# Kernel optimization log

Measured on AMD Instinct MI355X. Metric: run time of the kernel, lower is better.

## Reference

```python
import jax, jax.numpy as jnp
import numpy as np

B, M, H, NH = 64, 512, 1024, 8
HD = H // NH
EPS = 1e-5


def setup_inputs() -> dict:
    key = jax.random.key(0)
    ks = jax.random.split(key, 16)
    def n(k, shape, s=0.02):
        return jax.random.normal(k, shape, dtype=jnp.float32) * s
    z = lambda shape: jnp.zeros(shape, jnp.float32)
    return {
        "x": jax.random.normal(ks[0], (B, M, M), dtype=jnp.float32),
        # 1x1 Conv2d(1->H): weight [H,1,1,1] flattened to [H], plus bias [H]
        "conv_w": n(ks[1], (H,)), "conv_b": n(ks[2], (H,)),
        # MLP: Linear(M->H), ReLU, Linear(H->H); weights stored [in,out]
        "w1": n(ks[3], (M, H)), "b1": z((H,)),
        "w2": n(ks[4], (H, H)), "b2": z((H,)),
        "ln_g": jnp.ones((H,), jnp.float32), "ln_b": z((H,)),
        "wq": n(ks[5], (H, H)), "bq": z((H,)),
        "wk": n(ks[6], (H, H)), "bk": z((H,)),
        "wv": n(ks[7], (H, H)), "bv": z((H,)),
        "wo": n(ks[8], (H, H)), "bo": z((H,)),
        "wp": n(ks[9], (H, H)), "bp": z((H,)),
    }


def reference(x, conv_w, conv_b, w1, b1, w2, b2, ln_g, ln_b,
              wq, bq, wk, bk, wv, bv, wo, bo, wp, bp):
    # RegionConvolution: 1x1 conv over 1 input channel to H channels, then
    # mean over channels. Since mean_c(x*w_c + b_c) = x*mean(w) + mean(b),
    # compute the reduced affine form (identical math, no [B,H,M,M] temp).
    x = x + (x * conv_w.mean() + conv_b.mean())          # residual conv add, [B,M,M]
    # RegionEmbeddingMLP
    x_reg = jnp.maximum(x @ w1 + b1, 0.0) @ w2 + b2      # [B,M,H]
    # LayerNorm
    mu = x_reg.mean(-1, keepdims=True)
    var = ((x_reg - mu) ** 2).mean(-1, keepdims=True)
    x_norm = (x_reg - mu) / jnp.sqrt(var + EPS) * ln_g + ln_b
    # MHSA with multiplicative off-diagonal mask (diagonal scores zeroed)
    def heads(y):
        return y.reshape(B, M, NH, HD).transpose(0, 2, 1, 3)  # [B,NH,M,HD]
    q = heads(x_norm @ wq + bq)
    k = heads(x_norm @ wk + bk)
    v = heads(x_norm @ wv + bv)
    scores = jnp.einsum('bhqd,bhkd->bhqk', q, k) / jnp.sqrt(jnp.float32(HD))
    scores = scores * (1.0 - jnp.eye(M, dtype=scores.dtype))  # zero diagonal
    attn = jax.nn.softmax(scores, axis=-1)
    ctx = jnp.einsum('bhqk,bhkd->bhqd', attn, v)
    ctx = ctx.transpose(0, 2, 1, 3).reshape(B, M, H)
    attn_out = ctx @ wo + bo
    attn_out = attn_out @ wp + bp                        # output_proj
    return attn_out + x_reg                              # residual, [B,M,H]
```

## Files before the change

### kernel.cpp

```cpp
#include <hip/hip_runtime.h>
#include <hip/hip_fp16.h>
#include <cstdint>
#include <cstddef>

typedef _Float16 f16;
typedef _Float16 f16x8 __attribute__((ext_vector_type(8)));
typedef _Float16 f16x4 __attribute__((ext_vector_type(4)));
typedef float f32x4 __attribute__((ext_vector_type(4)));

#define NB 64
#define SEQ 512
#define HDIM 1024
#define NHEAD 8
#define HD 128
#define MR (NB * SEQ)
#define QK_LD 2048

__device__ __forceinline__ void async_copy16(const f16* g, f16* l) {
  __builtin_amdgcn_global_load_lds(
      (__attribute__((address_space(1))) void*)(void*)const_cast<f16*>(g),
      (__attribute__((address_space(3))) void*)l, 16, 0, 0);
}


__global__ __launch_bounds__(256) void conv_reduce(
    const float* __restrict__ cw, const float* __restrict__ cb,
    float* __restrict__ out2) {
  int t = threadIdx.x;
  float a = 0.f, b = 0.f;
  for (int i = t; i < HDIM; i += 256) { a += cw[i]; b += cb[i]; }
  for (int m = 32; m >= 1; m >>= 1) { a += __shfl_xor(a, m); b += __shfl_xor(b, m); }
  __shared__ float sa[4], sb[4];
  if ((t & 63) == 0) { sa[t >> 6] = a; sb[t >> 6] = b; }
  __syncthreads();
  if (t == 0) {
    out2[0] = (sa[0] + sa[1] + sa[2] + sa[3]) * (1.f / HDIM);
    out2[1] = (sb[0] + sb[1] + sb[2] + sb[3]) * (1.f / HDIM);
  }
}

__global__ __launch_bounds__(256) void prep_x(
    const float* __restrict__ x, const float* __restrict__ cs,
    f16* __restrict__ xh) {
  size_t i = (size_t)blockIdx.x * 256 + threadIdx.x;
  float cw = 1.f + cs[0], cb = cs[1];
  float4 v = ((const float4*)x)[i];
  f16x4 o;
  o[0] = (f16)(v.x * cw + cb);
  o[1] = (f16)(v.y * cw + cb);
  o[2] = (f16)(v.z * cw + cb);
  o[3] = (f16)(v.w * cw + cb);
  ((f16x4*)xh)[i] = o;
}

__global__ __launch_bounds__(256) void concat_bias(
    const float* __restrict__ bq, const float* __restrict__ bk,
    const float* __restrict__ bv, float* __restrict__ dst) {
  int i = blockIdx.x * 256 + threadIdx.x;
  if (i < 1024) dst[i] = bq[i];
  else if (i < 2048) dst[i] = bk[i - 1024];
  else dst[i] = bv[i - 2048];
}

__global__ __launch_bounds__(256) void cast_f16(
    const float* __restrict__ src, f16* __restrict__ dst) {
  size_t i = (size_t)blockIdx.x * 256 + threadIdx.x;
  float4 v = ((const float4*)src)[i];
  f16x4 o;
  o[0] = (f16)v.x; o[1] = (f16)v.y; o[2] = (f16)v.z; o[3] = (f16)v.w;
  ((f16x4*)dst)[i] = o;
}

__global__ __launch_bounds__(256) void fuse_bias_p1(
    const float* __restrict__ bo, const float* __restrict__ wp,
    float* __restrict__ partial) {
  int n = blockIdx.x * 256 + threadIdx.x;
  int jc = blockIdx.y;
  float s = 0.f;
#pragma unroll 8
  for (int j = jc * 128; j < jc * 128 + 128; j++) s += bo[j] * wp[(size_t)j * 1024 + n];
  partial[(size_t)jc * 1024 + n] = s;
}

__global__ __launch_bounds__(256) void fuse_bias_p2(
    const float* __restrict__ partial, const float* __restrict__ bp,
    float* __restrict__ bp2) {
  int n = blockIdx.x * 256 + threadIdx.x;
  float s = bp[n];
#pragma unroll
  for (int jc = 0; jc < 8; jc++) s += partial[(size_t)jc * 1024 + n];
  bp2[n] = s;
}

__global__ __launch_bounds__(256) void transpose_cast(
    const float* __restrict__ src, f16* __restrict__ dst, int K, int N) {
  __shared__ float tile[32][33];
  int tx = threadIdx.x, ty = threadIdx.y;
  int n0 = blockIdx.x * 32, k0 = blockIdx.y * 32;
#pragma unroll
  for (int r = 0; r < 32; r += 8) tile[ty + r][tx] = src[(size_t)(k0 + ty + r) * N + n0 + tx];
  __syncthreads();
#pragma unroll
  for (int r = 0; r < 32; r += 8)
    dst[(size_t)(n0 + ty + r) * K + k0 + tx] = (f16)tile[tx][ty + r];
}

__global__ __launch_bounds__(256) void transpose_cast5(
    const float* s0, const float* s1, const float* s2, const float* s3, const float* s4,
    f16* d0, f16* d1, f16* d2, f16* d3, f16* d4) {
  const float* src; f16* dst;
  switch (blockIdx.z) {
    case 0: src = s0; dst = d0; break;
    case 1: src = s1; dst = d1; break;
    case 2: src = s2; dst = d2; break;
    case 3: src = s3; dst = d3; break;
    default: src = s4; dst = d4; break;
  }
  __shared__ float tile[32][33];
  int tx = threadIdx.x, ty = threadIdx.y;
  int n0 = blockIdx.x * 32, k0 = blockIdx.y * 32;
#pragma unroll
  for (int r = 0; r < 32; r += 8) tile[ty + r][tx] = src[(size_t)(k0 + ty + r) * 1024 + n0 + tx];
  __syncthreads();
#pragma unroll
  for (int r = 0; r < 32; r += 8)
    dst[(size_t)(n0 + ty + r) * 1024 + k0 + tx] = (f16)tile[tx][ty + r];
}

__global__ __launch_bounds__(256) void ln_kernel(
    const f16* __restrict__ xin, const float* __restrict__ g,
    const float* __restrict__ bta, f16* __restrict__ out) {
  int row = blockIdx.x;
  int t = threadIdx.x;
  f16x4 vh = ((const f16x4*)(xin + (size_t)row * HDIM))[t];
  float vx = (float)vh[0], vy = (float)vh[1], vz = (float)vh[2], vw = (float)vh[3];
  float s = vx + vy + vz + vw;
  float s2 = vx * vx + vy * vy + vz * vz + vw * vw;
  for (int m = 32; m >= 1; m >>= 1) { s += __shfl_xor(s, m); s2 += __shfl_xor(s2, m); }
  __shared__ float sa[4], sb[4];
  if ((t & 63) == 0) { sa[t >> 6] = s; sb[t >> 6] = s2; }
  __syncthreads();
  float S = sa[0] + sa[1] + sa[2] + sa[3];
  float S2 = sb[0] + sb[1] + sb[2] + sb[3];
  float mu = S * (1.f / HDIM);
  float var = S2 * (1.f / HDIM) - mu * mu;
  float inv = rsqrtf(var + 1e-5f);
  float4 gv = ((const float4*)g)[t];
  float4 bv = ((const float4*)bta)[t];
  f16x4 o;
  o[0] = (f16)((vx - mu) * inv * gv.x + bv.x);
  o[1] = (f16)((vy - mu) * inv * gv.y + bv.y);
  o[2] = (f16)((vz - mu) * inv * gv.z + bv.z);
  o[3] = (f16)((vw - mu) * inv * gv.w + bv.w);
  ((f16x4*)(out + (size_t)row * HDIM))[t] = o;
}

template <int EPI>
__global__ __launch_bounds__(512) void gemm_nt(
    const f16* __restrict__ A, const f16* __restrict__ BT,
    const float* __restrict__ bias, void* __restrict__ Cout, int N, int K,
    const f16* __restrict__ Xres, f16* __restrict__ vTout) {
  __shared__ __align__(16) f16 As[128 * 64];
  __shared__ __align__(16) f16 Bs[128 * 64];
  const int tid = threadIdx.x;
  const int wave = tid >> 6, lane = tid & 63;
  const int l15 = lane & 15, quad = lane >> 4;

  const int gn = N >> 7;
  const int gm = (int)gridDim.x / gn;
  const int pid = blockIdx.x;
  const int npg = 16 * gn;
  const int gid = pid / npg;
  const int rem = pid - gid * npg;
  const int grows = min(16, gm - gid * 16);
  const int bm = gid * 16 + rem % grows;
  const int bn = rem / grows;

  const int wm = wave >> 2, wn = wave & 3;

  f32x4 z4 = {0.f, 0.f, 0.f, 0.f};
  f32x4 acc[4][2];
#pragma unroll
  for (int i = 0; i < 4; i++)
#pragma unroll
    for (int j = 0; j < 2; j++) acc[i][j] = z4;

  const int srow = tid >> 3;
  const int c = ((tid & 7) - (srow & 7)) & 7;
  const f16* Ag = A + (size_t)(bm * 128 + srow) * K + c * 8;
  const f16* Bg = BT + (size_t)(bn * 128 + srow) * K + c * 8;
  f16* Al0 = As + tid * 8;
  f16* Al1 = As + 64 * 64 + tid * 8;
  f16* Bl0 = Bs + tid * 8;
  f16* Bl1 = Bs + 64 * 64 + tid * 8;
  const size_t kstep = (size_t)64 * K;

  const int r7 = l15 & 7;

  for (int k0 = 0; k0 < K; k0 += 64) {
    async_copy16(Ag, Al0);
    async_copy16(Ag + kstep, Al1);
    async_copy16(Bg, Bl0);
    async_copy16(Bg + kstep, Bl1);
    Ag += 64; Bg += 64;
    __syncthreads();
#pragma unroll
    for (int s = 0; s < 2; s++) {
      f16x8 af[4], bfr[2];
#pragma unroll
      for (int t = 0; t < 4; t++) {
        int phys = (s * 4 + quad + r7) & 7;
        af[t] = *(const f16x8*)&As[(wm * 64 + t * 16 + l15) * 64 + phys * 8];
      }
#pragma unroll
      for (int u = 0; u < 2; u++) {
        int phys = (s * 4 + quad + r7) & 7;
        bfr[u] = *(const f16x8*)&Bs[(wn * 32 + u * 16 + l15) * 64 + phys * 8];
      }
#pragma unroll
      for (int i = 0; i < 4; i++)
#pragma unroll
        for (int j = 0; j < 2; j++)
          acc[i][j] = __builtin_amdgcn_mfma_f32_16x16x32_f16(af[i], bfr[j], acc[i][j], 0, 0, 0);
    }
    __syncthreads();
  }

  float* Cf = (float*)Cout;
  f16* Ch = (f16*)Cout;
#pragma unroll
  for (int i = 0; i < 4; i++) {
    int r0 = bm * 128 + wm * 64 + i * 16 + quad * 4;
#pragma unroll
    for (int j = 0; j < 2; j++) {
      int c0 = bn * 128 + wn * 32 + j * 16;
      int cc = c0 + l15;
      float bv = (EPI == 4) ? 0.f : bias[cc];
      if (EPI == 6 && c0 >= 2048) {
        int hh = (cc - 2048) >> 7, d = (cc - 2048) & 127;
        int bb = r0 >> 9, ml = r0 & 511;
        f16x4 o;
#pragma unroll
        for (int reg = 0; reg < 4; reg++) o[reg] = (f16)(acc[i][j][reg] + bv);
        *(f16x4*)&vTout[((size_t)(bb * NHEAD + hh) * HD + d) * SEQ + ml] = o;
      } else {
#pragma unroll
        for (int reg = 0; reg < 4; reg++) {
          float v = acc[i][j][reg] + bv;
          if (EPI == 0)      Ch[(size_t)(r0 + reg) * N + cc] = (f16)fmaxf(v, 0.f);
          else if (EPI == 1) Ch[(size_t)(r0 + reg) * N + cc] = (f16)v;
          else if (EPI == 4) Ch[(size_t)(r0 + reg) * N + cc] = (f16)v;
          else if (EPI == 5) {
            size_t idx = (size_t)(r0 + reg) * N + cc;
            Cf[idx] = v + (float)Xres[idx];
          } else {
            Ch[(size_t)(r0 + reg) * QK_LD + cc] = (f16)v;
          }
        }
      }
    }
  }
}

__global__ __launch_bounds__(512) void attn_kernel(
    const f16* __restrict__ qkv, const f16* __restrict__ vT,
    f16* __restrict__ ctx) {
  const int tid = threadIdx.x;
  const int wave = tid >> 6, lane = tid & 63;
  const int l15 = lane & 15, quad = lane >> 4;
  const int bidx = blockIdx.x;
  const int qc = bidx >> 9;
  const int bh = bidx & 511;
  const int h = bh & 7, bb = bh >> 3;

  const f16* Qbase = qkv + (size_t)(bb * SEQ) * QK_LD + h * 128;
  const f16* Kbase = Qbase + 1024;
  const f16* VTbase = vT + (size_t)(bb * NHEAD + h) * HD * SEQ;

  __shared__ __align__(16) f16 Ks[64 * 128];
  __shared__ __align__(16) f16 VTs[128 * 64];
  __shared__ __align__(16) f16 Ps[8 * 32 * 72];

  const float scale = 0.08838834764831845f;
  const int qrow0 = qc * 256 + wave * 32;
  f16x8 qf[2][4];
#pragma unroll
  for (int tm = 0; tm < 2; tm++)
#pragma unroll
    for (int s = 0; s < 4; s++) {
      qf[tm][s] = *(const f16x8*)(Qbase + (size_t)(qrow0 + tm * 16 + l15) * QK_LD + s * 32 + quad * 8);
#pragma unroll
      for (int e = 0; e < 8; e++) qf[tm][s][e] *= (f16)scale;
    }

  f32x4 z4 = {0.f, 0.f, 0.f, 0.f};
  f32x4 O[2][8];
#pragma unroll
  for (int i = 0; i < 2; i++)
#pragma unroll
    for (int j = 0; j < 8; j++) O[i][j] = z4;
  float lrow[2][4];
#pragma unroll
  for (int i = 0; i < 2; i++)
#pragma unroll
    for (int r = 0; r < 4; r++) lrow[i][r] = 0.f;

  const int kc = ((tid & 15) - ((tid >> 4) & 15)) & 15;
  const f16* Kg = Kbase + (size_t)(tid >> 4) * QK_LD + kc * 8;
  f16* Kl = Ks + tid * 8;
  const int vc = ((tid & 7) - ((tid >> 3) & 7)) & 7;
  const f16* Vg = VTbase + (size_t)(tid >> 3) * SEQ + vc * 8;
  f16* Vl = VTs + tid * 8;

  f16* Pw = &Ps[wave * 32 * 72];
  const int r7 = l15 & 7;

  for (int kt = 0; kt < 8; kt++) {
    const int krow0 = kt * 64;
#pragma unroll
    for (int i = 0; i < 2; i++)
      async_copy16(Kg + (size_t)(krow0 + 32 * i) * QK_LD, Kl + 4096 * i);
#pragma unroll
    for (int i = 0; i < 2; i++)
      async_copy16(Vg + (size_t)(64 * i) * SEQ + krow0, Vl + 4096 * i);
    __syncthreads();

    f32x4 S[2][4];
#pragma unroll
    for (int i = 0; i < 2; i++)
#pragma unroll
      for (int j = 0; j < 4; j++) S[i][j] = z4;
#pragma unroll
    for (int s = 0; s < 4; s++) {
      f16x8 bfr[4];
#pragma unroll
      for (int tn = 0; tn < 4; tn++) {
        int phys = (s * 4 + quad + l15) & 15;
        bfr[tn] = *(const f16x8*)&Ks[(tn * 16 + l15) * 128 + phys * 8];
      }
#pragma unroll
      for (int tm = 0; tm < 2; tm++)
#pragma unroll
        for (int tn = 0; tn < 4; tn++)
          S[tm][tn] = __builtin_amdgcn_mfma_f32_16x16x32_f16(qf[tm][s], bfr[tn], S[tm][tn], 0, 0, 0);
    }

#pragma unroll
    for (int tm = 0; tm < 2; tm++) {
#pragma unroll
      for (int reg = 0; reg < 4; reg++) {
        int qg = qrow0 + tm * 16 + quad * 4 + reg;
        float rs = 0.f;
#pragma unroll
        for (int tn = 0; tn < 4; tn++) {
          int kg = krow0 + tn * 16 + l15;
          float p = (kg == qg) ? 1.f : __expf(S[tm][tn][reg]);
          S[tm][tn][reg] = p;
          rs += p;
        }
        rs += __shfl_xor(rs, 1); rs += __shfl_xor(rs, 2);
        rs += __shfl_xor(rs, 4); rs += __shfl_xor(rs, 8);
        lrow[tm][reg] += rs;
      }
    }

#pragma unroll
    for (int tm = 0; tm < 2; tm++)
#pragma unroll
      for (int reg = 0; reg < 4; reg++)
#pragma unroll
        for (int tn = 0; tn < 4; tn++)
          Pw[(tm * 16 + quad * 4 + reg) * 72 + tn * 16 + l15] = (f16)S[tm][tn][reg];
    asm volatile("s_waitcnt lgkmcnt(0)" ::: "memory");

#pragma unroll
    for (int ks = 0; ks < 2; ks++) {
      f16x8 pa[2];
#pragma unroll
      for (int tm = 0; tm < 2; tm++)
        pa[tm] = *(const f16x8*)&Pw[(tm * 16 + l15) * 72 + ks * 32 + quad * 8];
#pragma unroll
      for (int tn = 0; tn < 8; tn++) {
        int phys = (ks * 4 + quad + r7) & 7;
        f16x8 vb = *(const f16x8*)&VTs[(tn * 16 + l15) * 64 + phys * 8];
#pragma unroll
        for (int tm = 0; tm < 2; tm++)
          O[tm][tn] = __builtin_amdgcn_mfma_f32_16x16x32_f16(pa[tm], vb, O[tm][tn], 0, 0, 0);
      }
    }
    __syncthreads();
  }

#pragma unroll
  for (int tm = 0; tm < 2; tm++)
#pragma unroll
    for (int reg = 0; reg < 4; reg++) {
      float inv = 1.f / lrow[tm][reg];
      int row = bb * SEQ + qrow0 + tm * 16 + quad * 4 + reg;
#pragma unroll
      for (int tn = 0; tn < 8; tn++) {
        int col = h * 128 + tn * 16 + l15;
        ctx[(size_t)row * HDIM + col] = (f16)(O[tm][tn][reg] * inv);
      }
    }
}


extern "C" void kernel_launch(void* const* d_in, const int* in_sizes, int n_in,
                              void* d_out, int out_size, void* d_ws, size_t ws_size,
                              hipStream_t stream) {
  (void)in_sizes; (void)n_in; (void)out_size; (void)ws_size;
  const float* x      = (const float*)d_in[0];
  const float* conv_w = (const float*)d_in[1];
  const float* conv_b = (const float*)d_in[2];
  const float* w1     = (const float*)d_in[3];
  const float* b1     = (const float*)d_in[4];
  const float* w2     = (const float*)d_in[5];
  const float* b2     = (const float*)d_in[6];
  const float* ln_g   = (const float*)d_in[7];
  const float* ln_b   = (const float*)d_in[8];
  const float* wq     = (const float*)d_in[9];
  const float* bq     = (const float*)d_in[10];
  const float* wk     = (const float*)d_in[11];
  const float* bk     = (const float*)d_in[12];
  const float* wv     = (const float*)d_in[13];
  const float* bv     = (const float*)d_in[14];
  const float* wo     = (const float*)d_in[15];
  const float* bo     = (const float*)d_in[16];
  const float* wp     = (const float*)d_in[17];
  const float* bp     = (const float*)d_in[18];
  float* out = (float*)d_out;

  char* ws = (char*)d_ws;
  size_t off = 0;
  auto alloc = [&](size_t bytes) {
    char* p = ws + off;
    off += (bytes + 255) & ~(size_t)255;
    return p;
  };
  float* cs    = (float*)alloc(8);
  f16* w1T     = (f16*)alloc((size_t)1024 * 512 * 2);
  f16* w2T     = (f16*)alloc((size_t)1024 * 1024 * 2);
  f16* qkvT    = (f16*)alloc((size_t)3072 * 1024 * 2);
  f16* wpT     = (f16*)alloc((size_t)1024 * 1024 * 2);
  f16* woh     = (f16*)alloc((size_t)1024 * 1024 * 2);
  f16* woPT    = (f16*)alloc((size_t)1024 * 1024 * 2);
  float* bqkv  = (float*)alloc((size_t)3072 * 4);
  float* bp2   = (float*)alloc((size_t)1024 * 4);
  float* part  = (float*)alloc((size_t)8 * 1024 * 4);
  f16* qkvQK   = (f16*)alloc((size_t)MR * QK_LD * 2);
  f16* h1      = (f16*)alloc((size_t)MR * 1024 * 2);
  f16* x_norm  = (f16*)alloc((size_t)MR * 1024 * 2);
  f16* x_regh  = (f16*)alloc((size_t)MR * 1024 * 2);
  f16* xh = qkvQK;
  f16* vT = h1;
  f16* ctx = x_norm;

  dim3 tb(32, 8);
  conv_reduce<<<1, 256, 0, stream>>>(conv_w, conv_b, cs);
  transpose_cast<<<dim3(32, 16), tb, 0, stream>>>(w1, w1T, 512, 1024);
  transpose_cast5<<<dim3(32, 32, 5), tb, 0, stream>>>(
      w2, wq, wk, wv, wp,
      w2T, qkvT, qkvT + (size_t)1024 * 1024, qkvT + (size_t)2048 * 1024, wpT);
  cast_f16<<<1024, 256, 0, stream>>>(wo, woh);
  concat_bias<<<12, 256, 0, stream>>>(bq, bk, bv, bqkv);
  fuse_bias_p1<<<dim3(4, 8), 256, 0, stream>>>(bo, wp, part);
  fuse_bias_p2<<<4, 256, 0, stream>>>(part, bp, bp2);
  prep_x<<<16384, 256, 0, stream>>>(x, cs, xh);

  gemm_nt<4><<<dim3(64), 512, 0, stream>>>(wpT, woh, nullptr, (void*)woPT, 1024, 1024, nullptr, nullptr);

  gemm_nt<0><<<dim3(256 * 8), 512, 0, stream>>>(xh, w1T, b1, (void*)h1, 1024, 512, nullptr, nullptr);
  gemm_nt<1><<<dim3(256 * 8), 512, 0, stream>>>(h1, w2T, b2, (void*)x_regh, 1024, 1024, nullptr, nullptr);
  ln_kernel<<<32768, 256, 0, stream>>>(x_regh, ln_g, ln_b, x_norm);
  gemm_nt<6><<<dim3(256 * 24), 512, 0, stream>>>(x_norm, qkvT, bqkv, (void*)qkvQK, 3072, 1024, nullptr, vT);
  attn_kernel<<<1024, 512, 0, stream>>>(qkvQK, vT, ctx);
  gemm_nt<5><<<dim3(256 * 8), 512, 0, stream>>>(ctx, woPT, bp2, (void*)out, 1024, 1024, x_regh, nullptr);
}
```

Before: 896.8 us.

## Add 256x256-tile pipelined GEMM kernel with XCD-aware block remap for main GEMMs

```diff
diff --git a/kernel.cpp b/kernel.cpp
--- a/kernel.cpp
+++ b/kernel.cpp
@@ -226,7 +226,6 @@
     __syncthreads();
   }
 
-  float* Cf = (float*)Cout;
   f16* Ch = (f16*)Cout;
 #pragma unroll
   for (int i = 0; i < 4; i++) {
@@ -236,6 +235,132 @@
       int c0 = bn * 128 + wn * 32 + j * 16;
       int cc = c0 + l15;
       float bv = (EPI == 4) ? 0.f : bias[cc];
+#pragma unroll
+      for (int reg = 0; reg < 4; reg++) {
+        float v = acc[i][j][reg] + bv;
+        Ch[(size_t)(r0 + reg) * N + cc] = (f16)v;
+      }
+    }
+  }
+  (void)Xres; (void)vTout;
+}
+
+template <int EPI>
+__global__ __launch_bounds__(512, 2) void gemm256(
+    const f16* __restrict__ A, const f16* __restrict__ BT,
+    const float* __restrict__ bias, void* __restrict__ Cout, int N, int K,
+    const f16* __restrict__ Xres, f16* __restrict__ vTout) {
+  __shared__ __align__(16) f16 As[4 * 8192];
+  __shared__ __align__(16) f16 Bs[4 * 8192];
+  const int tid = threadIdx.x;
+  const int wave = tid >> 6, lane = tid & 63;
+  const int l15 = lane & 15, quad = lane >> 4;
+  const int wm = wave >> 2, wn = wave & 3;
+
+  const int nbn = N >> 8;
+  const int nwg = (int)gridDim.x;
+  const int wg = (blockIdx.x & 7) * (nwg >> 3) + (blockIdx.x >> 3);
+  const int bm = wg / nbn, bn = wg - bm * nbn;
+
+  const int srow = tid >> 2;
+  const int sq = ((tid & 3) - (srow >> 1)) & 3;
+  const f16* Ag = A + (size_t)(bm * 256 + srow) * K + sq * 8;
+  const f16* Bg = BT + (size_t)(bn * 256 + srow) * K + sq * 8;
+  const size_t rstep = (size_t)128 * K;
+  const int rphys = ((quad + (l15 >> 1)) & 3) * 8;
+
+#define STAGE_A_(BUF, S, K0) do {                                      \
+    const f16* g_ = Ag + (K0) + (S) * 32;                              \
+    f16* l_ = As + ((BUF) * 2 + (S)) * 8192 + tid * 8;                 \
+    async_copy16(g_, l_); async_copy16(g_ + rstep, l_ + 4096); } while (0)
+#define STAGE_B_(BUF, S, K0) do {                                      \
+    const f16* g_ = Bg + (K0) + (S) * 32;                              \
+    f16* l_ = Bs + ((BUF) * 2 + (S)) * 8192 + tid * 8;                 \
+    async_copy16(g_, l_); async_copy16(g_ + rstep, l_ + 4096); } while (0)
+#define READ_A_(DST, BUF, S, RG) do {                                  \
+    _Pragma("unroll") for (int i_ = 0; i_ < 4; i_++)                   \
+      DST[i_] = *(const f16x8*)&As[((BUF) * 2 + (S)) * 8192 +          \
+          (wm * 128 + (RG) * 64 + i_ * 16 + l15) * 32 + rphys];        \
+  } while (0)
+#define READ_B_(DST, BUF, S) do {                                      \
+    _Pragma("unroll") for (int j_ = 0; j_ < 4; j_++)                   \
+      DST[j_] = *(const f16x8*)&Bs[((BUF) * 2 + (S)) * 8192 +          \
+          (wn * 64 + j_ * 16 + l15) * 32 + rphys];                     \
+  } while (0)
+#define MFMA16_(RG, AF, BF) do {                                       \
+    _Pragma("unroll") for (int i_ = 0; i_ < 4; i_++)                   \
+      _Pragma("unroll") for (int j_ = 0; j_ < 4; j_++)                 \
+        acc[(RG) * 4 + i_][j_] = __builtin_amdgcn_mfma_f32_16x16x32_f16( \
+            AF[i_], BF[j_], acc[(RG) * 4 + i_][j_], 0, 0, 0);          \
+  } while (0)
+#define BAR_() __builtin_amdgcn_s_barrier()
+#define LGKM0_() asm volatile("s_waitcnt lgkmcnt(0)" ::: "memory")
+#define VMC4_() asm volatile("s_waitcnt vmcnt(4)" ::: "memory")
+#define VMC0_() asm volatile("s_waitcnt vmcnt(0)" ::: "memory")
+
+  f32x4 z4 = {0.f, 0.f, 0.f, 0.f};
+  f32x4 acc[8][4];
+#pragma unroll
+  for (int i = 0; i < 8; i++)
+#pragma unroll
+    for (int j = 0; j < 4; j++) acc[i][j] = z4;
+
+  STAGE_A_(0, 0, 0); STAGE_B_(0, 0, 0); STAGE_A_(0, 1, 0); STAGE_B_(0, 1, 0);
+  VMC4_();
+  BAR_();
+
+  const int NT = K >> 6;
+  for (int t = 0; t < NT; ++t) {
+    const int buf = t & 1, bufn = buf ^ 1;
+    const int k1 = (t + 1) << 6;
+    const bool pf = (t + 1) < NT;
+    f16x8 af[4], bf0[4], bf1[4];
+
+    READ_A_(af, buf, 0, 0);
+    READ_B_(bf0, buf, 0);
+    if (pf) STAGE_A_(bufn, 0, k1);
+    BAR_(); LGKM0_();
+    __builtin_amdgcn_s_setprio(1);
+    MFMA16_(0, af, bf0);
+    __builtin_amdgcn_s_setprio(0);
+    BAR_();
+
+    READ_A_(af, buf, 0, 1);
+    if (pf) { STAGE_B_(bufn, 0, k1); VMC4_(); } else { VMC0_(); }
+    BAR_(); LGKM0_();
+    __builtin_amdgcn_s_setprio(1);
+    MFMA16_(1, af, bf0);
+    __builtin_amdgcn_s_setprio(0);
+    BAR_();
+
+    READ_A_(af, buf, 1, 0);
+    READ_B_(bf1, buf, 1);
+    if (pf) STAGE_A_(bufn, 1, k1);
+    BAR_(); LGKM0_();
+    __builtin_amdgcn_s_setprio(1);
+    MFMA16_(0, af, bf1);
+    __builtin_amdgcn_s_setprio(0);
+    BAR_();
+
+    READ_A_(af, buf, 1, 1);
+    if (pf) { STAGE_B_(bufn, 1, k1); VMC4_(); }
+    BAR_(); LGKM0_();
+    __builtin_amdgcn_s_setprio(1);
+    MFMA16_(1, af, bf1);
+    __builtin_amdgcn_s_setprio(0);
+    BAR_();
+  }
+
+  float* Cf = (float*)Cout;
+  f16* Ch = (f16*)Cout;
+#pragma unroll
+  for (int i = 0; i < 8; i++) {
+    int r0 = bm * 256 + wm * 128 + i * 16 + quad * 4;
+#pragma unroll
+    for (int j = 0; j < 4; j++) {
+      int c0 = bn * 256 + wn * 64 + j * 16;
+      int cc = c0 + l15;
+      float bv = bias[cc];
       if (EPI == 6 && c0 >= 2048) {
         int hh = (cc - 2048) >> 7, d = (cc - 2048) & 127;
         int bb = r0 >> 9, ml = r0 & 511;
@@ -249,7 +374,6 @@
           float v = acc[i][j][reg] + bv;
           if (EPI == 0)      Ch[(size_t)(r0 + reg) * N + cc] = (f16)fmaxf(v, 0.f);
           else if (EPI == 1) Ch[(size_t)(r0 + reg) * N + cc] = (f16)v;
-          else if (EPI == 4) Ch[(size_t)(r0 + reg) * N + cc] = (f16)v;
           else if (EPI == 5) {
             size_t idx = (size_t)(r0 + reg) * N + cc;
             Cf[idx] = v + (float)Xres[idx];
@@ -260,6 +384,15 @@
       }
     }
   }
+#undef STAGE_A_
+#undef STAGE_B_
+#undef READ_A_
+#undef READ_B_
+#undef MFMA16_
+#undef BAR_
+#undef LGKM0_
+#undef VMC4_
+#undef VMC0_
 }
 
 __global__ __launch_bounds__(512) void attn_kernel(
@@ -470,10 +603,10 @@
 
   gemm_nt<4><<<dim3(64), 512, 0, stream>>>(wpT, woh, nullptr, (void*)woPT, 1024, 1024, nullptr, nullptr);
 
-  gemm_nt<0><<<dim3(256 * 8), 512, 0, stream>>>(xh, w1T, b1, (void*)h1, 1024, 512, nullptr, nullptr);
-  gemm_nt<1><<<dim3(256 * 8), 512, 0, stream>>>(h1, w2T, b2, (void*)x_regh, 1024, 1024, nullptr, nullptr);
+  gemm256<0><<<dim3(128 * 4), 512, 0, stream>>>(xh, w1T, b1, (void*)h1, 1024, 512, nullptr, nullptr);
+  gemm256<1><<<dim3(128 * 4), 512, 0, stream>>>(h1, w2T, b2, (void*)x_regh, 1024, 1024, nullptr, nullptr);
   ln_kernel<<<32768, 256, 0, stream>>>(x_regh, ln_g, ln_b, x_norm);
-  gemm_nt<6><<<dim3(256 * 24), 512, 0, stream>>>(x_norm, qkvT, bqkv, (void*)qkvQK, 3072, 1024, nullptr, vT);
+  gemm256<6><<<dim3(128 * 12), 512, 0, stream>>>(x_norm, qkvT, bqkv, (void*)qkvQK, 3072, 1024, nullptr, vT);
   attn_kernel<<<1024, 512, 0, stream>>>(qkvQK, vT, ctx);
-  gemm_nt<5><<<dim3(256 * 8), 512, 0, stream>>>(ctx, woPT, bp2, (void*)out, 1024, 1024, x_regh, nullptr);
-}
+  gemm256<5><<<dim3(128 * 4), 512, 0, stream>>>(ctx, woPT, bp2, (void*)out, 1024, 1024, x_regh, nullptr);
+}
```

Result: no change. 881.9 us (-1.7%).

## Use 4-wave 64x64 warp tiles in GEMM, split QKV GEMM, add MFMA priority

Applied to the files above, without the earlier changes.

```diff
diff --git a/kernel.cpp b/kernel.cpp
--- a/kernel.cpp
+++ b/kernel.cpp
@@ -156,7 +156,7 @@
 }
 
 template <int EPI>
-__global__ __launch_bounds__(512) void gemm_nt(
+__global__ __launch_bounds__(256) void gemm_nt(
     const f16* __restrict__ A, const f16* __restrict__ BT,
     const float* __restrict__ bias, void* __restrict__ Cout, int N, int K,
     const f16* __restrict__ Xres, f16* __restrict__ vTout) {
@@ -176,51 +176,44 @@
   const int bm = gid * 16 + rem % grows;
   const int bn = rem / grows;
 
-  const int wm = wave >> 2, wn = wave & 3;
+  const int wm = wave >> 1, wn = wave & 1;
 
   f32x4 z4 = {0.f, 0.f, 0.f, 0.f};
-  f32x4 acc[4][2];
+  f32x4 acc[4][4];
 #pragma unroll
   for (int i = 0; i < 4; i++)
 #pragma unroll
-    for (int j = 0; j < 2; j++) acc[i][j] = z4;
+    for (int j = 0; j < 4; j++) acc[i][j] = z4;
 
   const int srow = tid >> 3;
   const int c = ((tid & 7) - (srow & 7)) & 7;
   const f16* Ag = A + (size_t)(bm * 128 + srow) * K + c * 8;
   const f16* Bg = BT + (size_t)(bn * 128 + srow) * K + c * 8;
-  f16* Al0 = As + tid * 8;
-  f16* Al1 = As + 64 * 64 + tid * 8;
-  f16* Bl0 = Bs + tid * 8;
-  f16* Bl1 = Bs + 64 * 64 + tid * 8;
-  const size_t kstep = (size_t)64 * K;
+  const size_t kstep32 = (size_t)32 * K;
 
   const int r7 = l15 & 7;
 
   for (int k0 = 0; k0 < K; k0 += 64) {
-    async_copy16(Ag, Al0);
-    async_copy16(Ag + kstep, Al1);
-    async_copy16(Bg, Bl0);
-    async_copy16(Bg + kstep, Bl1);
+#pragma unroll
+    for (int i = 0; i < 4; i++) async_copy16(Ag + i * kstep32, As + i * 2048 + tid * 8);
+#pragma unroll
+    for (int i = 0; i < 4; i++) async_copy16(Bg + i * kstep32, Bs + i * 2048 + tid * 8);
     Ag += 64; Bg += 64;
     __syncthreads();
 #pragma unroll
     for (int s = 0; s < 2; s++) {
-      f16x8 af[4], bfr[2];
-#pragma unroll
-      for (int t = 0; t < 4; t++) {
-        int phys = (s * 4 + quad + r7) & 7;
+      const int phys = (s * 4 + quad + r7) & 7;
+      f16x8 af[4], bfr[4];
+#pragma unroll
+      for (int t = 0; t < 4; t++)
         af[t] = *(const f16x8*)&As[(wm * 64 + t * 16 + l15) * 64 + phys * 8];
-      }
-#pragma unroll
-      for (int u = 0; u < 2; u++) {
-        int phys = (s * 4 + quad + r7) & 7;
-        bfr[u] = *(const f16x8*)&Bs[(wn * 32 + u * 16 + l15) * 64 + phys * 8];
-      }
+#pragma unroll
+      for (int u = 0; u < 4; u++)
+        bfr[u] = *(const f16x8*)&Bs[(wn * 64 + u * 16 + l15) * 64 + phys * 8];
 #pragma unroll
       for (int i = 0; i < 4; i++)
 #pragma unroll
-        for (int j = 0; j < 2; j++)
+        for (int j = 0; j < 4; j++)
           acc[i][j] = __builtin_amdgcn_mfma_f32_16x16x32_f16(af[i], bfr[j], acc[i][j], 0, 0, 0);
     }
     __syncthreads();
@@ -232,12 +225,12 @@
   for (int i = 0; i < 4; i++) {
     int r0 = bm * 128 + wm * 64 + i * 16 + quad * 4;
 #pragma unroll
-    for (int j = 0; j < 2; j++) {
-      int c0 = bn * 128 + wn * 32 + j * 16;
+    for (int j = 0; j < 4; j++) {
+      int c0 = bn * 128 + wn * 64 + j * 16;
       int cc = c0 + l15;
       float bv = (EPI == 4) ? 0.f : bias[cc];
-      if (EPI == 6 && c0 >= 2048) {
-        int hh = (cc - 2048) >> 7, d = (cc - 2048) & 127;
+      if (EPI == 7) {
+        int hh = cc >> 7, d = cc & 127;
         int bb = r0 >> 9, ml = r0 & 511;
         f16x4 o;
 #pragma unroll
@@ -253,8 +246,6 @@
           else if (EPI == 5) {
             size_t idx = (size_t)(r0 + reg) * N + cc;
             Cf[idx] = v + (float)Xres[idx];
-          } else {
-            Ch[(size_t)(r0 + reg) * QK_LD + cc] = (f16)v;
           }
         }
       }
@@ -338,11 +329,13 @@
         int phys = (s * 4 + quad + l15) & 15;
         bfr[tn] = *(const f16x8*)&Ks[(tn * 16 + l15) * 128 + phys * 8];
       }
+      __builtin_amdgcn_s_setprio(1);
 #pragma unroll
       for (int tm = 0; tm < 2; tm++)
 #pragma unroll
         for (int tn = 0; tn < 4; tn++)
           S[tm][tn] = __builtin_amdgcn_mfma_f32_16x16x32_f16(qf[tm][s], bfr[tn], S[tm][tn], 0, 0, 0);
+      __builtin_amdgcn_s_setprio(0);
     }
 
 #pragma unroll
@@ -379,6 +372,7 @@
 #pragma unroll
       for (int tm = 0; tm < 2; tm++)
         pa[tm] = *(const f16x8*)&Pw[(tm * 16 + l15) * 72 + ks * 32 + quad * 8];
+      __builtin_amdgcn_s_setprio(1);
 #pragma unroll
       for (int tn = 0; tn < 8; tn++) {
         int phys = (ks * 4 + quad + r7) & 7;
@@ -387,6 +381,7 @@
         for (int tm = 0; tm < 2; tm++)
           O[tm][tn] = __builtin_amdgcn_mfma_f32_16x16x32_f16(pa[tm], vb, O[tm][tn], 0, 0, 0);
       }
+      __builtin_amdgcn_s_setprio(0);
     }
     __syncthreads();
   }
@@ -468,12 +463,14 @@
   fuse_bias_p2<<<4, 256, 0, stream>>>(part, bp, bp2);
   prep_x<<<16384, 256, 0, stream>>>(x, cs, xh);
 
-  gemm_nt<4><<<dim3(64), 512, 0, stream>>>(wpT, woh, nullptr, (void*)woPT, 1024, 1024, nullptr, nullptr);
-
-  gemm_nt<0><<<dim3(256 * 8), 512, 0, stream>>>(xh, w1T, b1, (void*)h1, 1024, 512, nullptr, nullptr);
-  gemm_nt<1><<<dim3(256 * 8), 512, 0, stream>>>(h1, w2T, b2, (void*)x_regh, 1024, 1024, nullptr, nullptr);
+  gemm_nt<4><<<dim3(64), 256, 0, stream>>>(wpT, woh, nullptr, (void*)woPT, 1024, 1024, nullptr, nullptr);
+
+  gemm_nt<0><<<dim3(256 * 8), 256, 0, stream>>>(xh, w1T, b1, (void*)h1, 1024, 512, nullptr, nullptr);
+  gemm_nt<1><<<dim3(256 * 8), 256, 0, stream>>>(h1, w2T, b2, (void*)x_regh, 1024, 1024, nullptr, nullptr);
   ln_kernel<<<32768, 256, 0, stream>>>(x_regh, ln_g, ln_b, x_norm);
-  gemm_nt<6><<<dim3(256 * 24), 512, 0, stream>>>(x_norm, qkvT, bqkv, (void*)qkvQK, 3072, 1024, nullptr, vT);
+  gemm_nt<1><<<dim3(256 * 16), 256, 0, stream>>>(x_norm, qkvT, bqkv, (void*)qkvQK, 2048, 1024, nullptr, nullptr);
+  gemm_nt<7><<<dim3(256 * 8), 256, 0, stream>>>(x_norm, qkvT + (size_t)2048 * 1024, bqkv + 2048,
+                                                nullptr, 1024, 1024, nullptr, vT);
   attn_kernel<<<1024, 512, 0, stream>>>(qkvQK, vT, ctx);
-  gemm_nt<5><<<dim3(256 * 8), 512, 0, stream>>>(ctx, woPT, bp2, (void*)out, 1024, 1024, x_regh, nullptr);
-}
+  gemm_nt<5><<<dim3(256 * 8), 256, 0, stream>>>(ctx, woPT, bp2, (void*)out, 1024, 1024, x_regh, nullptr);
+}
```

Result: slower. 916.7 us (+2.2%).

## Compute transposed QK scores and pass P to PV MFMA via register permutes

Applied to the files above, without the earlier changes.

```diff
diff --git a/kernel.cpp b/kernel.cpp
--- a/kernel.cpp
+++ b/kernel.cpp
@@ -6,7 +6,9 @@
 typedef _Float16 f16;
 typedef _Float16 f16x8 __attribute__((ext_vector_type(8)));
 typedef _Float16 f16x4 __attribute__((ext_vector_type(4)));
+typedef _Float16 f16x2 __attribute__((ext_vector_type(2)));
 typedef float f32x4 __attribute__((ext_vector_type(4)));
+typedef unsigned int ui4 __attribute__((ext_vector_type(4)));
 
 #define NB 64
 #define SEQ 512
@@ -279,7 +281,6 @@
 
   __shared__ __align__(16) f16 Ks[64 * 128];
   __shared__ __align__(16) f16 VTs[128 * 64];
-  __shared__ __align__(16) f16 Ps[8 * 32 * 72];
 
   const float scale = 0.08838834764831845f;
   const int qrow0 = qc * 256 + wave * 32;
@@ -299,11 +300,7 @@
   for (int i = 0; i < 2; i++)
 #pragma unroll
     for (int j = 0; j < 8; j++) O[i][j] = z4;
-  float lrow[2][4];
-#pragma unroll
-  for (int i = 0; i < 2; i++)
-#pragma unroll
-    for (int r = 0; r < 4; r++) lrow[i][r] = 0.f;
+  float lrow[2] = {0.f, 0.f};
 
   const int kc = ((tid & 15) - ((tid >> 4) & 15)) & 15;
   const f16* Kg = Kbase + (size_t)(tid >> 4) * QK_LD + kc * 8;
@@ -312,8 +309,8 @@
   const f16* Vg = VTbase + (size_t)(tid >> 3) * SEQ + vc * 8;
   f16* Vl = VTs + tid * 8;
 
-  f16* Pw = &Ps[wave * 32 * 72];
   const int r7 = l15 & 7;
+  const bool qodd = (quad & 1) != 0;
 
   for (int kt = 0; kt < 8; kt++) {
     const int krow0 = kt * 64;
@@ -325,11 +322,11 @@
       async_copy16(Vg + (size_t)(64 * i) * SEQ + krow0, Vl + 4096 * i);
     __syncthreads();
 
-    f32x4 S[2][4];
-#pragma unroll
-    for (int i = 0; i < 2; i++)
-#pragma unroll
-      for (int j = 0; j < 4; j++) S[i][j] = z4;
+    f32x4 ST[4][2];
+#pragma unroll
+    for (int i = 0; i < 4; i++)
+#pragma unroll
+      for (int j = 0; j < 2; j++) ST[i][j] = z4;
 #pragma unroll
     for (int s = 0; s < 4; s++) {
       f16x8 bfr[4];
@@ -338,55 +335,73 @@
         int phys = (s * 4 + quad + l15) & 15;
         bfr[tn] = *(const f16x8*)&Ks[(tn * 16 + l15) * 128 + phys * 8];
       }
-#pragma unroll
-      for (int tm = 0; tm < 2; tm++)
-#pragma unroll
-        for (int tn = 0; tn < 4; tn++)
-          S[tm][tn] = __builtin_amdgcn_mfma_f32_16x16x32_f16(qf[tm][s], bfr[tn], S[tm][tn], 0, 0, 0);
-    }
-
+      __builtin_amdgcn_s_setprio(1);
+#pragma unroll
+      for (int tn = 0; tn < 4; tn++)
+#pragma unroll
+        for (int tm = 0; tm < 2; tm++)
+          ST[tn][tm] = __builtin_amdgcn_mfma_f32_16x16x32_f16(bfr[tn], qf[tm][s], ST[tn][tm], 0, 0, 0);
+      __builtin_amdgcn_s_setprio(0);
+    }
+
+    f16x8 pa[2][2];
 #pragma unroll
     for (int tm = 0; tm < 2; tm++) {
-#pragma unroll
-      for (int reg = 0; reg < 4; reg++) {
-        int qg = qrow0 + tm * 16 + quad * 4 + reg;
-        float rs = 0.f;
-#pragma unroll
-        for (int tn = 0; tn < 4; tn++) {
-          int kg = krow0 + tn * 16 + l15;
-          float p = (kg == qg) ? 1.f : __expf(S[tm][tn][reg]);
-          S[tm][tn][reg] = p;
-          rs += p;
+      const int qg = qrow0 + tm * 16 + l15;
+      float rs = 0.f;
+      unsigned int H[4][2];
+#pragma unroll
+      for (int tn = 0; tn < 4; tn++) {
+        float p[4];
+#pragma unroll
+        for (int reg = 0; reg < 4; reg++) {
+          int kg = krow0 + tn * 16 + quad * 4 + reg;
+          float v = (kg == qg) ? 1.f : __expf(ST[tn][tm][reg]);
+          p[reg] = v;
+          rs += v;
         }
-        rs += __shfl_xor(rs, 1); rs += __shfl_xor(rs, 2);
-        rs += __shfl_xor(rs, 4); rs += __shfl_xor(rs, 8);
-        lrow[tm][reg] += rs;
-      }
-    }
-
-#pragma unroll
-    for (int tm = 0; tm < 2; tm++)
-#pragma unroll
-      for (int reg = 0; reg < 4; reg++)
-#pragma unroll
-        for (int tn = 0; tn < 4; tn++)
-          Pw[(tm * 16 + quad * 4 + reg) * 72 + tn * 16 + l15] = (f16)S[tm][tn][reg];
-    asm volatile("s_waitcnt lgkmcnt(0)" ::: "memory");
+        f16x2 h01 = {(f16)p[0], (f16)p[1]};
+        f16x2 h23 = {(f16)p[2], (f16)p[3]};
+        H[tn][0] = __builtin_bit_cast(unsigned int, h01);
+        H[tn][1] = __builtin_bit_cast(unsigned int, h23);
+      }
+      rs += __shfl_xor(rs, 16);
+      rs += __shfl_xor(rs, 32);
+      lrow[tm] += rs;
+
+#pragma unroll
+      for (int ks = 0; ks < 2; ks++) {
+        unsigned int a0 = H[ks * 2][0], a1 = H[ks * 2][1];
+        unsigned int b0 = H[ks * 2 + 1][0], b1 = H[ks * 2 + 1][1];
+        asm volatile("s_nop 1\n\tv_permlane32_swap_b32 %0, %1\n\ts_nop 1"
+                     : "+v"(a0), "+v"(b0));
+        asm volatile("s_nop 1\n\tv_permlane32_swap_b32 %0, %1\n\ts_nop 1"
+                     : "+v"(a1), "+v"(b1));
+        unsigned int c0 = (unsigned int)__shfl_xor((int)a0, 16);
+        unsigned int c1 = (unsigned int)__shfl_xor((int)a1, 16);
+        unsigned int d0 = (unsigned int)__shfl_xor((int)b0, 16);
+        unsigned int d1 = (unsigned int)__shfl_xor((int)b1, 16);
+        ui4 wv;
+        wv[0] = qodd ? d0 : a0;
+        wv[1] = qodd ? d1 : a1;
+        wv[2] = qodd ? b0 : c0;
+        wv[3] = qodd ? b1 : c1;
+        pa[tm][ks] = __builtin_bit_cast(f16x8, wv);
+      }
+    }
 
 #pragma unroll
     for (int ks = 0; ks < 2; ks++) {
-      f16x8 pa[2];
-#pragma unroll
-      for (int tm = 0; tm < 2; tm++)
-        pa[tm] = *(const f16x8*)&Pw[(tm * 16 + l15) * 72 + ks * 32 + quad * 8];
+      __builtin_amdgcn_s_setprio(1);
 #pragma unroll
       for (int tn = 0; tn < 8; tn++) {
         int phys = (ks * 4 + quad + r7) & 7;
         f16x8 vb = *(const f16x8*)&VTs[(tn * 16 + l15) * 64 + phys * 8];
 #pragma unroll
         for (int tm = 0; tm < 2; tm++)
-          O[tm][tn] = __builtin_amdgcn_mfma_f32_16x16x32_f16(pa[tm], vb, O[tm][tn], 0, 0, 0);
-      }
+          O[tm][tn] = __builtin_amdgcn_mfma_f32_16x16x32_f16(pa[tm][ks], vb, O[tm][tn], 0, 0, 0);
+      }
+      __builtin_amdgcn_s_setprio(0);
     }
     __syncthreads();
   }
@@ -395,7 +410,8 @@
   for (int tm = 0; tm < 2; tm++)
 #pragma unroll
     for (int reg = 0; reg < 4; reg++) {
-      float inv = 1.f / lrow[tm][reg];
+      float lv = __shfl(lrow[tm], quad * 4 + reg);
+      float inv = 1.f / lv;
       int row = bb * SEQ + qrow0 + tm * 16 + quad * 4 + reg;
 #pragma unroll
       for (int tn = 0; tn < 8; tn++) {
```

New measurement: 854.2 us. 1.05x faster.
